# Kernel optimization log

Hardware: AMD Instinct MI355X
Metric: run time of the kernel (lower is better)

Reference implementation:

```python
import jax, jax.numpy as jnp
import numpy as np
import math

B, L, DIM = 2, 2048, 2048
N_HEADS, N_KV = 16, 4
HD = DIM // N_HEADS          # 128
N_REP = N_HEADS // N_KV      # 4
THETA = 10000.0


def setup_inputs() -> dict:
    key = jax.random.key(0)
    ks = jax.random.split(key, 6)
    x = jax.random.normal(ks[0], (B, L, DIM), dtype=jnp.float32)
    # rotary phasor freqs_cis = exp(i * t * inv_freq), stored as cos/sin
    inv_freq = 1.0 / (THETA ** (jnp.arange(0, HD, 2, dtype=jnp.float32) / HD))  # [HD//2]
    ang = jnp.arange(L, dtype=jnp.float32)[:, None] * inv_freq[None, :]          # [L, HD//2]
    freqs_cos = jnp.cos(ang)
    freqs_sin = jnp.sin(ang)
    s = 0.02
    wq = jax.random.normal(ks[1], (DIM, DIM), dtype=jnp.float32) * s
    wk = jax.random.normal(ks[2], (N_KV * HD, DIM), dtype=jnp.float32) * s
    wv = jax.random.normal(ks[3], (N_KV * HD, DIM), dtype=jnp.float32) * s
    wo = jax.random.normal(ks[4], (DIM, DIM), dtype=jnp.float32) * s
    return {"x": x, "freqs_cos": freqs_cos, "freqs_sin": freqs_sin,
            "wq": wq, "wk": wk, "wv": wv, "wo": wo}


def _apply_rope(t, cos, sin):
    # t: [B, L, H, HD]; cos/sin: [L, HD//2] -> broadcast [1, L, 1, HD//2]
    tr = t.reshape(*t.shape[:-1], HD // 2, 2)
    t0, t1 = tr[..., 0], tr[..., 1]
    c = cos[None, :, None, :]
    s = sin[None, :, None, :]
    r0 = t0 * c - t1 * s
    r1 = t0 * s + t1 * c
    return jnp.stack([r0, r1], axis=-1).reshape(t.shape)


def reference(x, freqs_cos, freqs_sin, wq, wk, wv, wo):
    Bx, Lx, _ = x.shape
    xq = (x @ wq.T).reshape(Bx, Lx, N_HEADS, HD)
    xk = (x @ wk.T).reshape(Bx, Lx, N_KV, HD)
    xv = (x @ wv.T).reshape(Bx, Lx, N_KV, HD)
    xq = _apply_rope(xq, freqs_cos, freqs_sin)
    xk = _apply_rope(xk, freqs_cos, freqs_sin)
    # repeat_kv (GQA expansion) then [B, H, L, HD]
    keys = jnp.repeat(xk, N_REP, axis=2).transpose(0, 2, 1, 3)
    values = jnp.repeat(xv, N_REP, axis=2).transpose(0, 2, 1, 3)
    q = xq.transpose(0, 2, 1, 3)
    scores = jnp.einsum('bhqd,bhkd->bhqk', q, keys) / math.sqrt(HD)
    mask = jnp.triu(jnp.full((Lx, Lx), -jnp.inf, dtype=scores.dtype), k=1)
    scores = scores + mask[None, None]
    probs = jax.nn.softmax(scores.astype(jnp.float32), axis=-1).astype(q.dtype)
    out = jnp.einsum('bhqk,bhkd->bhqd', probs, values)
    out = out.transpose(0, 2, 1, 3).reshape(Bx, Lx, -1)
    output = out @ wo.T
    return (output, keys, values)
```

## Files before the change

kernel.cpp:

```cpp
#include <hip/hip_runtime.h>
#include <hip/hip_bf16.h>

using bf16x8 = __attribute__((ext_vector_type(8))) short;
using f32x4  = __attribute__((ext_vector_type(4))) float;

__device__ __forceinline__ unsigned short f32_to_bf16(float f) {
  unsigned u = __float_as_uint(f);
  u += 0x7FFFu + ((u >> 16) & 1u);
  return (unsigned short)(u >> 16);
}
__device__ __forceinline__ unsigned pack2(float lo, float hi) {
  __hip_bfloat162 h = __float22bfloat162_rn(make_float2(lo, hi));
  return *reinterpret_cast<unsigned*>(&h);
}
__device__ __forceinline__ void gload_lds16(const void* g, void* l) {
  __builtin_amdgcn_global_load_lds(
      (const __attribute__((address_space(1))) unsigned int*)g,
      (__attribute__((address_space(3))) unsigned int*)l, 16, 0, 0);
}

__global__ void cast_bf16_kernel(const float* __restrict__ src,
                                 unsigned short* __restrict__ dst) {
  int i = blockIdx.x * blockDim.x + threadIdx.x;
  float4 v = reinterpret_cast<const float4*>(src)[i];
  ushort4 o;
  o.x = f32_to_bf16(v.x); o.y = f32_to_bf16(v.y);
  o.z = f32_to_bf16(v.z); o.w = f32_to_bf16(v.w);
  reinterpret_cast<ushort4*>(dst)[i] = o;
}
__global__ void cast2_bf16_kernel(const float* __restrict__ s0, unsigned short* __restrict__ d0,
                                  int n0v, const float* __restrict__ s1,
                                  unsigned short* __restrict__ d1) {
  int i = blockIdx.x * blockDim.x + threadIdx.x;
  const float* s; unsigned short* d; int j;
  if (i < n0v) { s = s0; d = d0; j = i; } else { s = s1; d = d1; j = i - n0v; }
  float4 v = reinterpret_cast<const float4*>(s)[j];
  ushort4 o;
  o.x = f32_to_bf16(v.x); o.y = f32_to_bf16(v.y);
  o.z = f32_to_bf16(v.z); o.w = f32_to_bf16(v.w);
  reinterpret_cast<ushort4*>(d)[j] = o;
}

template <int BM>
__global__ __launch_bounds__(512, 2) void gemm256_kernel(
    const unsigned short* __restrict__ A, const unsigned short* __restrict__ Bw,
    float* __restrict__ C, int M, int N, int K) {
  constexpr int ABYTES = BM * 128;
  constexpr int BBYTES = 256 * 128;
  constexpr int BUFB   = ABYTES + BBYTES;
  constexpr int ALOADS = BM / 64;
  constexpr int WROWS  = BM / 32;
  __shared__ __align__(16) char Lsh[2 * BUFB];

  const int tid = threadIdx.x;
  const int wid = tid >> 6, lane = tid & 63;
  const int lr = lane & 15, lg = lane >> 4;
  const int wr = wid >> 2, wc = wid & 3;
  const int bn = blockIdx.x, bm = blockIdx.y;
  const int x0 = lg * 16;

  f32x4 acc[WROWS][4] = {};

  const char* Ag = (const char*)A + (size_t)(bm * BM) * K * 2;
  const char* Bg = (const char*)Bw + (size_t)(bn * 256) * K * 2;

  int aoff[ALOADS], boff[4];
#pragma unroll
  for (int i = 0; i < ALOADS; ++i) {
    int lin = wid * (BM * 16) + i * 1024 + lane * 16;
    int grow = lin >> 7;
    int gcol = (lin & 127) ^ ((grow & 7) << 4);
    aoff[i] = grow * (K * 2) + gcol;
  }
#pragma unroll
  for (int i = 0; i < 4; ++i) {
    int lin = wid * 4096 + i * 1024 + lane * 16;
    int grow = lin >> 7;
    int gcol = (lin & 127) ^ ((grow & 7) << 4);
    boff[i] = grow * (K * 2) + gcol;
  }

  auto stage = [&](int s, int buf) {
    const int kb = s * 128;
    char* Lb = Lsh + buf * BUFB;
#pragma unroll
    for (int i = 0; i < ALOADS; ++i)
      gload_lds16(Ag + aoff[i] + kb, Lb + wid * (BM * 16) + i * 1024);
#pragma unroll
    for (int i = 0; i < 4; ++i)
      gload_lds16(Bg + boff[i] + kb, Lb + ABYTES + wid * 4096 + i * 1024);
  };

  auto kstep = [&](char* Lb) {
    bf16x8 bfr[4][2];
#pragma unroll
    for (int fc = 0; fc < 4; ++fc) {
      const int row = wc * 64 + fc * 16 + lr;
      const int base = ABYTES + row * 128;
      const int sw = (row & 7) << 4;
#pragma unroll
      for (int ks = 0; ks < 2; ++ks)
        bfr[fc][ks] = *reinterpret_cast<const bf16x8*>(Lb + base + ((ks * 64 + x0) ^ sw));
    }
#pragma unroll
    for (int q = 0; q < WROWS / 2; ++q) {
      bf16x8 af[2][2];
#pragma unroll
      for (int t = 0; t < 2; ++t) {
        const int row = wr * (BM / 2) + (2 * q + t) * 16 + lr;
        const int base = row * 128;
        const int sw = (row & 7) << 4;
#pragma unroll
        for (int ks = 0; ks < 2; ++ks)
          af[t][ks] = *reinterpret_cast<const bf16x8*>(Lb + base + ((ks * 64 + x0) ^ sw));
      }
      asm volatile("s_waitcnt lgkmcnt(0)" ::: "memory");
      __builtin_amdgcn_sched_barrier(0);
      __builtin_amdgcn_s_setprio(1);
#pragma unroll
      for (int t = 0; t < 2; ++t)
#pragma unroll
        for (int fc = 0; fc < 4; ++fc) {
          acc[2 * q + t][fc] = __builtin_amdgcn_mfma_f32_16x16x32_bf16(af[t][0], bfr[fc][0], acc[2 * q + t][fc], 0, 0, 0);
          acc[2 * q + t][fc] = __builtin_amdgcn_mfma_f32_16x16x32_bf16(af[t][1], bfr[fc][1], acc[2 * q + t][fc], 0, 0, 0);
        }
      __builtin_amdgcn_s_setprio(0);
    }
  };

  const int NST = K >> 6;
  stage(0, 0);
  for (int it = 0; it < NST / 2; ++it) {
    __builtin_amdgcn_s_barrier();
    stage(2 * it + 1, 1);
    if constexpr (BM == 256) asm volatile("s_waitcnt vmcnt(8)" ::: "memory");
    else                     asm volatile("s_waitcnt vmcnt(6)" ::: "memory");
    __builtin_amdgcn_s_barrier();
    kstep(Lsh);
    __builtin_amdgcn_s_barrier();
    if (it < NST / 2 - 1) {
      stage(2 * it + 2, 0);
      if constexpr (BM == 256) asm volatile("s_waitcnt vmcnt(8)" ::: "memory");
      else                     asm volatile("s_waitcnt vmcnt(6)" ::: "memory");
    } else {
      asm volatile("s_waitcnt vmcnt(0)" ::: "memory");
    }
    __builtin_amdgcn_s_barrier();
    kstep(Lsh + BUFB);
  }

#pragma unroll
  for (int fr = 0; fr < WROWS; ++fr) {
    const int m = bm * BM + wr * (BM / 2) + fr * 16 + lg * 4;
#pragma unroll
    for (int fc = 0; fc < 4; ++fc) {
      const int n = bn * 256 + wc * 64 + fc * 16 + lr;
#pragma unroll
      for (int r = 0; r < 4; ++r)
        C[(size_t)(m + r) * N + n] = acc[fr][fc][r];
    }
  }
}

__global__ void rope_k_kernel(const float* __restrict__ xqkv, const float* __restrict__ fc,
                              const float* __restrict__ fs, unsigned short* __restrict__ kbf,
                              float* __restrict__ keys) {
  int idx = blockIdx.x * 256 + threadIdx.x;
  int i = idx & 63;
  int kvh = (idx >> 6) & 3;
  int l = (idx >> 8) & 2047;
  int b = idx >> 19;
  float2 t = reinterpret_cast<const float2*>(xqkv)[(size_t)(b * 2048 + l) * 1536 + 1024 + kvh * 64 + i];
  float c = fc[l * 64 + i], s = fs[l * 64 + i];
  float r0 = t.x * c - t.y * s;
  float r1 = t.x * s + t.y * c;
  int kidx = ((b * 4 + kvh) * 2048 + l) * 64 + i;
  ushort2 o; o.x = f32_to_bf16(r0); o.y = f32_to_bf16(r1);
  reinterpret_cast<ushort2*>(kbf)[kidx] = o;
  float2 f; f.x = r0; f.y = r1;
#pragma unroll
  for (int rep = 0; rep < 4; ++rep) {
    int h = kvh * 4 + rep;
    reinterpret_cast<float2*>(keys)[((b * 16 + h) * 2048 + l) * 64 + i] = f;
  }
}

__global__ void v_proc_kernel(const float* __restrict__ xqkv, unsigned short* __restrict__ vt,
                              float* __restrict__ values) {
  int idx = blockIdx.x * 256 + threadIdx.x;
  int d = idx & 127;
  int kvh = (idx >> 7) & 3;
  int l = (idx >> 9) & 2047;
  int b = idx >> 20;
  float v = xqkv[(size_t)(b * 2048 + l) * 3072 + 2560 + kvh * 128 + d];
#pragma unroll
  for (int rep = 0; rep < 4; ++rep) {
    int h = kvh * 4 + rep;
    values[((size_t)(b * 16 + h) * 2048 + l) * 128 + d] = v;
  }
  vt[((size_t)(b * 4 + kvh) * 128 + d) * 2048 + l] = f32_to_bf16(v);
}

__global__ __launch_bounds__(256) void attn_kernel(
    const float* __restrict__ xq, const float* __restrict__ fc,
    const float* __restrict__ fs, const unsigned short* __restrict__ kbf,
    const unsigned short* __restrict__ vt, unsigned short* __restrict__ obf) {
  __shared__ unsigned short Ks[64 * 128];
  __shared__ unsigned short Vs[128 * 64];
  const int tid = threadIdx.x;
  const int w = tid >> 6, lane = tid & 63;
  const int lr = lane & 15, lg = lane >> 4;
  const int bid = blockIdx.x;
  const int qt = 15 - (bid >> 5);
  const int bh = bid & 31;
  const int b = bh >> 4, h = bh & 15, kv = h >> 2;
  const float ALPHA = 0.12751791437664778f;
  const int swz = (lr & 7) << 4;

  const int qr0 = qt * 128 + w * 16 + lr;
  const int qr1 = qr0 + 64;

  bf16x8 qf[2][4];
#pragma unroll
  for (int t = 0; t < 2; ++t) {
    const int qrow = t ? qr1 : qr0;
    const float* xqp = xq + (size_t)(b * 2048 + qrow) * 3072 + h * 128;
    const float* fcp = fc + qrow * 64;
    const float* fsp = fs + qrow * 64;
#pragma unroll
    for (int s = 0; s < 4; ++s) {
      float4 f0 = *reinterpret_cast<const float4*>(xqp + s * 32 + lg * 8);
      float4 f1 = *reinterpret_cast<const float4*>(xqp + s * 32 + lg * 8 + 4);
      float4 c4 = *reinterpret_cast<const float4*>(fcp + s * 16 + lg * 4);
      float4 s4 = *reinterpret_cast<const float4*>(fsp + s * 16 + lg * 4);
      c4.x *= ALPHA; c4.y *= ALPHA; c4.z *= ALPHA; c4.w *= ALPHA;
      s4.x *= ALPHA; s4.y *= ALPHA; s4.z *= ALPHA; s4.w *= ALPHA;
      union { bf16x8 v8; unsigned u[4]; } uu;
      uu.u[0] = pack2(f0.x * c4.x - f0.y * s4.x, f0.x * s4.x + f0.y * c4.x);
      uu.u[1] = pack2(f0.z * c4.y - f0.w * s4.y, f0.z * s4.y + f0.w * c4.y);
      uu.u[2] = pack2(f1.x * c4.z - f1.y * s4.z, f1.x * s4.z + f1.y * c4.z);
      uu.u[3] = pack2(f1.z * c4.w - f1.w * s4.w, f1.z * s4.w + f1.w * c4.w);
      qf[t][s] = uu.v8;
    }
  }

  f32x4 acc[2][8] = {};
  float mrow[2] = {-1e30f, -1e30f}, lsum[2] = {0.f, 0.f};

  const char* kgbase = (const char*)(kbf + (size_t)(b * 4 + kv) * 2048 * 128);
  const char* vgbase = (const char*)(vt + (size_t)(b * 4 + kv) * 128 * 2048);

  int ksrc[4], vsrc[4];
#pragma unroll
  for (int i = 0; i < 4; ++i) {
    int p = w * 4096 + i * 1024 + lane * 16;
    int krow = p >> 8;
    int kperm = ((krow >> 5) << 5) + ((krow >> 4) & 1) + (((krow >> 2) & 3) << 3) + ((krow & 3) << 1);
    int kcol = (p & 255) ^ ((krow & 7) << 4);
    ksrc[i] = kperm * 256 + kcol;
    int drow = p >> 7;
    int dcol = (p & 127) ^ ((drow & 7) << 4);
    vsrc[i] = drow * 4096 + dcol;
  }

  auto softmax_t = [&](const f32x4* st, int t, bool mask, int qrow, int kb, bf16x8* pt) {
    float xv[4][4];
    float mt = -1e30f;
#pragma unroll
    for (int c = 0; c < 4; ++c)
#pragma unroll
      for (int r = 0; r < 4; ++r) {
        float v = st[c][r];
        if (mask) {
          int ka = kb + ((c >> 1) << 5) + (c & 1) + 8 * lg + 2 * r;
          v = (ka <= qrow) ? v : -1e30f;
        }
        xv[c][r] = v;
        mt = fmaxf(mt, v);
      }
    mt = fmaxf(mt, __shfl_xor(mt, 16));
    mt = fmaxf(mt, __shfl_xor(mt, 32));
    float facm = 1.0f;
    if (!__all(mt <= mrow[t] + 8.0f)) {
      float mnew = fmaxf(mrow[t], mt);
      facm = exp2f(mrow[t] - mnew);
      mrow[t] = mnew;
#pragma unroll
      for (int dt = 0; dt < 8; ++dt)
#pragma unroll
        for (int r = 0; r < 4; ++r) acc[t][dt][r] *= facm;
    }
    float rs = 0.f;
    float pv[4][4];
#pragma unroll
    for (int c = 0; c < 4; ++c)
#pragma unroll
      for (int r = 0; r < 4; ++r) {
        float p = exp2f(xv[c][r] - mrow[t]);
        pv[c][r] = p;
        rs += p;
      }
    rs += __shfl_xor(rs, 16);
    rs += __shfl_xor(rs, 32);
    lsum[t] = lsum[t] * facm + rs;
#pragma unroll
    for (int kk = 0; kk < 2; ++kk) {
      union { bf16x8 v8; unsigned u[4]; } uu;
#pragma unroll
      for (int wd = 0; wd < 4; ++wd)
        uu.u[wd] = pack2(pv[2 * kk][wd], pv[2 * kk + 1][wd]);
      pt[kk] = uu.v8;
    }
  };

  const int nst = 2 * qt + 2;
  for (int j = 0; j < nst; ++j) {
    const int kb = j * 64;
    __syncthreads();
    {
      const char* kg = kgbase + (size_t)kb * 256;
      const char* vg = vgbase + (size_t)kb * 2;
#pragma unroll
      for (int i = 0; i < 4; ++i) {
        gload_lds16(kg + ksrc[i], (char*)Ks + w * 4096 + i * 1024);
        gload_lds16(vg + vsrc[i], (char*)Vs + w * 4096 + i * 1024);
      }
    }
    __syncthreads();
    const bool only1 = (j == nst - 1);
    const bool do0 = !only1;
    const bool m0 = (j == nst - 2);
    const bool m1 = only1;
    f32x4 sT0[4], sT1[4];
#pragma unroll
    for (int c = 0; c < 4; ++c) {
      bf16x8 kf[4];
#pragma unroll
      for (int s = 0; s < 4; ++s)
        kf[s] = *reinterpret_cast<const bf16x8*>((char*)Ks + (((c * 16 + lr) * 256 + s * 64 + lg * 16) ^ swz));
      f32x4 t0 = {0.f, 0.f, 0.f, 0.f}, t1 = {0.f, 0.f, 0.f, 0.f};
#pragma unroll
      for (int s = 0; s < 4; ++s) {
        if (do0) t0 = __builtin_amdgcn_mfma_f32_16x16x32_bf16(kf[s], qf[0][s], t0, 0, 0, 0);
        t1 = __builtin_amdgcn_mfma_f32_16x16x32_bf16(kf[s], qf[1][s], t1, 0, 0, 0);
      }
      sT0[c] = t0; sT1[c] = t1;
    }
    bf16x8 pt0[2], pt1[2];
    if (do0) softmax_t(sT0, 0, m0, qr0, kb, pt0);
    softmax_t(sT1, 1, m1, qr1, kb, pt1);
#pragma unroll
    for (int dt = 0; dt < 8; ++dt) {
      bf16x8 v0 = *reinterpret_cast<const bf16x8*>((char*)Vs + (((dt * 16 + lr) * 128 + lg * 16) ^ swz));
      bf16x8 v1 = *reinterpret_cast<const bf16x8*>((char*)Vs + (((dt * 16 + lr) * 128 + 64 + lg * 16) ^ swz));
      if (do0) {
        acc[0][dt] = __builtin_amdgcn_mfma_f32_16x16x32_bf16(v0, pt0[0], acc[0][dt], 0, 0, 0);
        acc[0][dt] = __builtin_amdgcn_mfma_f32_16x16x32_bf16(v1, pt0[1], acc[0][dt], 0, 0, 0);
      }
      acc[1][dt] = __builtin_amdgcn_mfma_f32_16x16x32_bf16(v0, pt1[0], acc[1][dt], 0, 0, 0);
      acc[1][dt] = __builtin_amdgcn_mfma_f32_16x16x32_bf16(v1, pt1[1], acc[1][dt], 0, 0, 0);
    }
  }

#pragma unroll
  for (int t = 0; t < 2; ++t) {
    const int qrow = t ? qr1 : qr0;
    float inv = 1.0f / lsum[t];
#pragma unroll
    for (int dt = 0; dt < 8; ++dt) {
      ushort4 o;
      o.x = f32_to_bf16(acc[t][dt][0] * inv);
      o.y = f32_to_bf16(acc[t][dt][1] * inv);
      o.z = f32_to_bf16(acc[t][dt][2] * inv);
      o.w = f32_to_bf16(acc[t][dt][3] * inv);
      *reinterpret_cast<ushort4*>(obf + ((size_t)(b * 2048 + qrow)) * 2048 + h * 128 + dt * 16 + lg * 4) = o;
    }
  }
}

extern "C" void kernel_launch(void* const* d_in, const int* in_sizes, int n_in,
                              void* d_out, int out_size, void* d_ws, size_t ws_size,
                              hipStream_t stream) {
  const float* x  = (const float*)d_in[0];
  const float* fc = (const float*)d_in[1];
  const float* fs = (const float*)d_in[2];
  const float* wq = (const float*)d_in[3];
  const float* wk = (const float*)d_in[4];
  const float* wv = (const float*)d_in[5];
  const float* wo = (const float*)d_in[6];

  float* out    = (float*)d_out;
  float* keys   = out + 8388608;
  float* values = out + 16777216;

  char* ws = (char*)d_ws;
  unsigned short* WQKV = (unsigned short*)(ws + 0);
  unsigned short* WO   = (unsigned short*)(ws + 12582912);
  unsigned short* XBF  = (unsigned short*)(ws + 20971520);
  float*          XQKV = (float*)(ws + 37748736);
  unsigned short* KBF  = (unsigned short*)(ws + 88080384);
  unsigned short* VTB  = (unsigned short*)(ws + 92274688);
  unsigned short* ATT  = XBF;

  cast2_bf16_kernel<<<8192, 256, 0, stream>>>(wq, WQKV, 1048576, wo, WO);
  cast2_bf16_kernel<<<2048, 256, 0, stream>>>(wk, WQKV + 2048 * 2048, 262144,
                                              wv, WQKV + 2560 * 2048);
  cast_bf16_kernel<<<8192, 256, 0, stream>>>(x, XBF);

  gemm256_kernel<256><<<dim3(12, 16), 512, 0, stream>>>(XBF, WQKV, XQKV, 4096, 3072, 2048);

  rope_k_kernel<<<4096, 256, 0, stream>>>(XQKV, fc, fs, KBF, keys);
  v_proc_kernel<<<8192, 256, 0, stream>>>(XQKV, VTB, values);

  attn_kernel<<<512, 256, 0, stream>>>(XQKV, fc, fs, KBF, VTB, ATT);

  gemm256_kernel<128><<<dim3(8, 32), 512, 0, stream>>>(ATT, WO, out, 4096, 2048, 2048);
}
```

Measured before the change: 265.5 us.

## Fuse cast and KV-prep launches; restructure attention to read K/V directly from global

```diff
diff --git a/kernel.cpp b/kernel.cpp
--- a/kernel.cpp
+++ b/kernel.cpp
@@ -19,26 +19,24 @@
       (__attribute__((address_space(3))) unsigned int*)l, 16, 0, 0);
 }
 
-__global__ void cast_bf16_kernel(const float* __restrict__ src,
-                                 unsigned short* __restrict__ dst) {
+__global__ void cast_all_kernel(const float* __restrict__ wq, const float* __restrict__ wo,
+                                const float* __restrict__ wk, const float* __restrict__ wv,
+                                const float* __restrict__ x,
+                                unsigned short* __restrict__ WQKV,
+                                unsigned short* __restrict__ WO,
+                                unsigned short* __restrict__ XBF) {
   int i = blockIdx.x * blockDim.x + threadIdx.x;
-  float4 v = reinterpret_cast<const float4*>(src)[i];
+  const float4* s; ushort4* d; int j;
+  if (i < 1048576)      { s = (const float4*)wq; d = (ushort4*)WQKV;            j = i; }
+  else if (i < 2097152) { s = (const float4*)wo; d = (ushort4*)WO;              j = i - 1048576; }
+  else if (i < 2359296) { s = (const float4*)wk; d = (ushort4*)WQKV + 1048576;  j = i - 2097152; }
+  else if (i < 2621440) { s = (const float4*)wv; d = (ushort4*)WQKV + 1310720;  j = i - 2359296; }
+  else                  { s = (const float4*)x;  d = (ushort4*)XBF;             j = i - 2621440; }
+  float4 v = s[j];
   ushort4 o;
   o.x = f32_to_bf16(v.x); o.y = f32_to_bf16(v.y);
   o.z = f32_to_bf16(v.z); o.w = f32_to_bf16(v.w);
-  reinterpret_cast<ushort4*>(dst)[i] = o;
-}
-__global__ void cast2_bf16_kernel(const float* __restrict__ s0, unsigned short* __restrict__ d0,
-                                  int n0v, const float* __restrict__ s1,
-                                  unsigned short* __restrict__ d1) {
-  int i = blockIdx.x * blockDim.x + threadIdx.x;
-  const float* s; unsigned short* d; int j;
-  if (i < n0v) { s = s0; d = d0; j = i; } else { s = s1; d = d1; j = i - n0v; }
-  float4 v = reinterpret_cast<const float4*>(s)[j];
-  ushort4 o;
-  o.x = f32_to_bf16(v.x); o.y = f32_to_bf16(v.y);
-  o.z = f32_to_bf16(v.z); o.w = f32_to_bf16(v.w);
-  reinterpret_cast<ushort4*>(d)[j] = o;
+  d[j] = o;
 }
 
 template <int BM>
@@ -162,68 +160,64 @@
   }
 }
 
-__global__ void rope_k_kernel(const float* __restrict__ xqkv, const float* __restrict__ fc,
-                              const float* __restrict__ fs, unsigned short* __restrict__ kbf,
-                              float* __restrict__ keys) {
-  int idx = blockIdx.x * 256 + threadIdx.x;
-  int i = idx & 63;
-  int kvh = (idx >> 6) & 3;
-  int l = (idx >> 8) & 2047;
-  int b = idx >> 19;
-  float2 t = reinterpret_cast<const float2*>(xqkv)[(size_t)(b * 2048 + l) * 1536 + 1024 + kvh * 64 + i];
-  float c = fc[l * 64 + i], s = fs[l * 64 + i];
-  float r0 = t.x * c - t.y * s;
-  float r1 = t.x * s + t.y * c;
-  int kidx = ((b * 4 + kvh) * 2048 + l) * 64 + i;
-  ushort2 o; o.x = f32_to_bf16(r0); o.y = f32_to_bf16(r1);
-  reinterpret_cast<ushort2*>(kbf)[kidx] = o;
-  float2 f; f.x = r0; f.y = r1;
-#pragma unroll
-  for (int rep = 0; rep < 4; ++rep) {
-    int h = kvh * 4 + rep;
-    reinterpret_cast<float2*>(keys)[((b * 16 + h) * 2048 + l) * 64 + i] = f;
-  }
-}
-
-__global__ void v_proc_kernel(const float* __restrict__ xqkv, unsigned short* __restrict__ vt,
-                              float* __restrict__ values) {
-  int idx = blockIdx.x * 256 + threadIdx.x;
-  int d = idx & 127;
-  int kvh = (idx >> 7) & 3;
-  int l = (idx >> 9) & 2047;
-  int b = idx >> 20;
-  float v = xqkv[(size_t)(b * 2048 + l) * 3072 + 2560 + kvh * 128 + d];
-#pragma unroll
-  for (int rep = 0; rep < 4; ++rep) {
-    int h = kvh * 4 + rep;
-    values[((size_t)(b * 16 + h) * 2048 + l) * 128 + d] = v;
-  }
-  vt[((size_t)(b * 4 + kvh) * 128 + d) * 2048 + l] = f32_to_bf16(v);
+__global__ void kv_proc_kernel(const float* __restrict__ xqkv, const float* __restrict__ fc,
+                               const float* __restrict__ fs, unsigned short* __restrict__ kbf,
+                               float* __restrict__ keys, unsigned short* __restrict__ vt,
+                               float* __restrict__ values) {
+  int bid = blockIdx.x;
+  if (bid < 4096) {
+    int idx = bid * 256 + threadIdx.x;
+    int i = idx & 63;
+    int kvh = (idx >> 6) & 3;
+    int l = (idx >> 8) & 2047;
+    int b = idx >> 19;
+    float2 t = reinterpret_cast<const float2*>(xqkv)[(size_t)(b * 2048 + l) * 1536 + 1024 + kvh * 64 + i];
+    float c = fc[l * 64 + i], s = fs[l * 64 + i];
+    float r0 = t.x * c - t.y * s;
+    float r1 = t.x * s + t.y * c;
+    int kidx = ((b * 4 + kvh) * 2048 + l) * 64 + i;
+    ushort2 o; o.x = f32_to_bf16(r0); o.y = f32_to_bf16(r1);
+    reinterpret_cast<ushort2*>(kbf)[kidx] = o;
+    float2 f; f.x = r0; f.y = r1;
+#pragma unroll
+    for (int rep = 0; rep < 4; ++rep) {
+      int h = kvh * 4 + rep;
+      reinterpret_cast<float2*>(keys)[((b * 16 + h) * 2048 + l) * 64 + i] = f;
+    }
+  } else {
+    int idx = (bid - 4096) * 256 + threadIdx.x;
+    int d = idx & 127;
+    int kvh = (idx >> 7) & 3;
+    int l = (idx >> 9) & 2047;
+    int b = idx >> 20;
+    float v = xqkv[(size_t)(b * 2048 + l) * 3072 + 2560 + kvh * 128 + d];
+#pragma unroll
+    for (int rep = 0; rep < 4; ++rep) {
+      int h = kvh * 4 + rep;
+      values[((size_t)(b * 16 + h) * 2048 + l) * 128 + d] = v;
+    }
+    vt[((size_t)(b * 4 + kvh) * 128 + d) * 2048 + l] = f32_to_bf16(v);
+  }
 }
 
 __global__ __launch_bounds__(256) void attn_kernel(
     const float* __restrict__ xq, const float* __restrict__ fc,
     const float* __restrict__ fs, const unsigned short* __restrict__ kbf,
     const unsigned short* __restrict__ vt, unsigned short* __restrict__ obf) {
-  __shared__ unsigned short Ks[64 * 128];
-  __shared__ unsigned short Vs[128 * 64];
+  __shared__ unsigned short Pbuf[4][16 * 40];
   const int tid = threadIdx.x;
   const int w = tid >> 6, lane = tid & 63;
   const int lr = lane & 15, lg = lane >> 4;
   const int bid = blockIdx.x;
-  const int qt = 15 - (bid >> 5);
+  const int qpos = 31 - (bid >> 5);
   const int bh = bid & 31;
   const int b = bh >> 4, h = bh & 15, kv = h >> 2;
+  const int qbase = qpos * 64 + w * 16;
   const float ALPHA = 0.12751791437664778f;
-  const int swz = (lr & 7) << 4;
-
-  const int qr0 = qt * 128 + w * 16 + lr;
-  const int qr1 = qr0 + 64;
-
-  bf16x8 qf[2][4];
-#pragma unroll
-  for (int t = 0; t < 2; ++t) {
-    const int qrow = t ? qr1 : qr0;
+
+  bf16x8 qf[4];
+  {
+    const int qrow = qbase + lr;
     const float* xqp = xq + (size_t)(b * 2048 + qrow) * 3072 + h * 128;
     const float* fcp = fc + qrow * 64;
     const float* fsp = fs + qrow * 64;
@@ -240,140 +234,105 @@
       uu.u[1] = pack2(f0.z * c4.y - f0.w * s4.y, f0.z * s4.y + f0.w * c4.y);
       uu.u[2] = pack2(f1.x * c4.z - f1.y * s4.z, f1.x * s4.z + f1.y * c4.z);
       uu.u[3] = pack2(f1.z * c4.w - f1.w * s4.w, f1.z * s4.w + f1.w * c4.w);
-      qf[t][s] = uu.v8;
-    }
-  }
-
-  f32x4 acc[2][8] = {};
-  float mrow[2] = {-1e30f, -1e30f}, lsum[2] = {0.f, 0.f};
-
-  const char* kgbase = (const char*)(kbf + (size_t)(b * 4 + kv) * 2048 * 128);
-  const char* vgbase = (const char*)(vt + (size_t)(b * 4 + kv) * 128 * 2048);
-
-  int ksrc[4], vsrc[4];
-#pragma unroll
-  for (int i = 0; i < 4; ++i) {
-    int p = w * 4096 + i * 1024 + lane * 16;
-    int krow = p >> 8;
-    int kperm = ((krow >> 5) << 5) + ((krow >> 4) & 1) + (((krow >> 2) & 3) << 3) + ((krow & 3) << 1);
-    int kcol = (p & 255) ^ ((krow & 7) << 4);
-    ksrc[i] = kperm * 256 + kcol;
-    int drow = p >> 7;
-    int dcol = (p & 127) ^ ((drow & 7) << 4);
-    vsrc[i] = drow * 4096 + dcol;
-  }
-
-  auto softmax_t = [&](const f32x4* st, int t, bool mask, int qrow, int kb, bf16x8* pt) {
-    float xv[4][4];
-    float mt = -1e30f;
-#pragma unroll
-    for (int c = 0; c < 4; ++c)
+      qf[s] = uu.v8;
+    }
+  }
+
+  f32x4 acc[8] = {};
+  float mrow[4], lsum[4];
+#pragma unroll
+  for (int r = 0; r < 4; ++r) { mrow[r] = -1e30f; lsum[r] = 0.0f; }
+
+  const unsigned short* kbase_p = kbf + (size_t)(b * 4 + kv) * 2048 * 128;
+  const unsigned short* vbase_p = vt + (size_t)(b * 4 + kv) * 128 * 2048;
+
+  const int nblocks = (qbase + 47) >> 5;
+  for (int j = 0; j < nblocks; ++j) {
+    const int kb = j * 32;
+    f32x4 s0 = {0.f, 0.f, 0.f, 0.f}, s1 = {0.f, 0.f, 0.f, 0.f};
+    __builtin_amdgcn_s_setprio(1);
+#pragma unroll
+    for (int s = 0; s < 4; ++s) {
+      bf16x8 kf = *reinterpret_cast<const bf16x8*>(kbase_p + (size_t)(kb + lr) * 128 + s * 32 + lg * 8);
+      s0 = __builtin_amdgcn_mfma_f32_16x16x32_bf16(qf[s], kf, s0, 0, 0, 0);
+    }
+#pragma unroll
+    for (int s = 0; s < 4; ++s) {
+      bf16x8 kf = *reinterpret_cast<const bf16x8*>(kbase_p + (size_t)(kb + 16 + lr) * 128 + s * 32 + lg * 8);
+      s1 = __builtin_amdgcn_mfma_f32_16x16x32_bf16(qf[s], kf, s1, 0, 0, 0);
+    }
+    __builtin_amdgcn_s_setprio(0);
+    float v0[4], v1[4], rm[4];
+    bool okall = true;
+#pragma unroll
+    for (int r = 0; r < 4; ++r) {
+      int q = qbase + lg * 4 + r;
+      v0[r] = ((kb + lr) <= q) ? s0[r] : -1e30f;
+      v1[r] = ((kb + 16 + lr) <= q) ? s1[r] : -1e30f;
+      float m = fmaxf(v0[r], v1[r]);
+      m = fmaxf(m, __shfl_xor(m, 1));
+      m = fmaxf(m, __shfl_xor(m, 2));
+      m = fmaxf(m, __shfl_xor(m, 4));
+      m = fmaxf(m, __shfl_xor(m, 8));
+      rm[r] = m;
+      okall = okall && (m <= mrow[r] + 8.0f);
+    }
+    float p0[4], p1[4];
+    if (__all(okall)) {
 #pragma unroll
       for (int r = 0; r < 4; ++r) {
-        float v = st[c][r];
-        if (mask) {
-          int ka = kb + ((c >> 1) << 5) + (c & 1) + 8 * lg + 2 * r;
-          v = (ka <= qrow) ? v : -1e30f;
-        }
-        xv[c][r] = v;
-        mt = fmaxf(mt, v);
+        p0[r] = exp2f(v0[r] - mrow[r]);
+        p1[r] = exp2f(v1[r] - mrow[r]);
+        float rs = p0[r] + p1[r];
+        rs += __shfl_xor(rs, 1);
+        rs += __shfl_xor(rs, 2);
+        rs += __shfl_xor(rs, 4);
+        rs += __shfl_xor(rs, 8);
+        lsum[r] += rs;
       }
-    mt = fmaxf(mt, __shfl_xor(mt, 16));
-    mt = fmaxf(mt, __shfl_xor(mt, 32));
-    float facm = 1.0f;
-    if (!__all(mt <= mrow[t] + 8.0f)) {
-      float mnew = fmaxf(mrow[t], mt);
-      facm = exp2f(mrow[t] - mnew);
-      mrow[t] = mnew;
-#pragma unroll
-      for (int dt = 0; dt < 8; ++dt)
-#pragma unroll
-        for (int r = 0; r < 4; ++r) acc[t][dt][r] *= facm;
-    }
-    float rs = 0.f;
-    float pv[4][4];
-#pragma unroll
-    for (int c = 0; c < 4; ++c)
+    } else {
+      float fac[4];
 #pragma unroll
       for (int r = 0; r < 4; ++r) {
-        float p = exp2f(xv[c][r] - mrow[t]);
-        pv[c][r] = p;
-        rs += p;
+        float mnew = fmaxf(mrow[r], rm[r]);
+        fac[r] = exp2f(mrow[r] - mnew);
+        mrow[r] = mnew;
+        p0[r] = exp2f(v0[r] - mnew);
+        p1[r] = exp2f(v1[r] - mnew);
+        float rs = p0[r] + p1[r];
+        rs += __shfl_xor(rs, 1);
+        rs += __shfl_xor(rs, 2);
+        rs += __shfl_xor(rs, 4);
+        rs += __shfl_xor(rs, 8);
+        lsum[r] = lsum[r] * fac[r] + rs;
       }
-    rs += __shfl_xor(rs, 16);
-    rs += __shfl_xor(rs, 32);
-    lsum[t] = lsum[t] * facm + rs;
-#pragma unroll
-    for (int kk = 0; kk < 2; ++kk) {
-      union { bf16x8 v8; unsigned u[4]; } uu;
-#pragma unroll
-      for (int wd = 0; wd < 4; ++wd)
-        uu.u[wd] = pack2(pv[2 * kk][wd], pv[2 * kk + 1][wd]);
-      pt[kk] = uu.v8;
-    }
-  };
-
-  const int nst = 2 * qt + 2;
-  for (int j = 0; j < nst; ++j) {
-    const int kb = j * 64;
-    __syncthreads();
-    {
-      const char* kg = kgbase + (size_t)kb * 256;
-      const char* vg = vgbase + (size_t)kb * 2;
-#pragma unroll
-      for (int i = 0; i < 4; ++i) {
-        gload_lds16(kg + ksrc[i], (char*)Ks + w * 4096 + i * 1024);
-        gload_lds16(vg + vsrc[i], (char*)Vs + w * 4096 + i * 1024);
+#pragma unroll
+      for (int ft = 0; ft < 8; ++ft) {
+        acc[ft][0] *= fac[0]; acc[ft][1] *= fac[1];
+        acc[ft][2] *= fac[2]; acc[ft][3] *= fac[3];
       }
     }
-    __syncthreads();
-    const bool only1 = (j == nst - 1);
-    const bool do0 = !only1;
-    const bool m0 = (j == nst - 2);
-    const bool m1 = only1;
-    f32x4 sT0[4], sT1[4];
-#pragma unroll
-    for (int c = 0; c < 4; ++c) {
-      bf16x8 kf[4];
-#pragma unroll
-      for (int s = 0; s < 4; ++s)
-        kf[s] = *reinterpret_cast<const bf16x8*>((char*)Ks + (((c * 16 + lr) * 256 + s * 64 + lg * 16) ^ swz));
-      f32x4 t0 = {0.f, 0.f, 0.f, 0.f}, t1 = {0.f, 0.f, 0.f, 0.f};
-#pragma unroll
-      for (int s = 0; s < 4; ++s) {
-        if (do0) t0 = __builtin_amdgcn_mfma_f32_16x16x32_bf16(kf[s], qf[0][s], t0, 0, 0, 0);
-        t1 = __builtin_amdgcn_mfma_f32_16x16x32_bf16(kf[s], qf[1][s], t1, 0, 0, 0);
-      }
-      sT0[c] = t0; sT1[c] = t1;
-    }
-    bf16x8 pt0[2], pt1[2];
-    if (do0) softmax_t(sT0, 0, m0, qr0, kb, pt0);
-    softmax_t(sT1, 1, m1, qr1, kb, pt1);
-#pragma unroll
-    for (int dt = 0; dt < 8; ++dt) {
-      bf16x8 v0 = *reinterpret_cast<const bf16x8*>((char*)Vs + (((dt * 16 + lr) * 128 + lg * 16) ^ swz));
-      bf16x8 v1 = *reinterpret_cast<const bf16x8*>((char*)Vs + (((dt * 16 + lr) * 128 + 64 + lg * 16) ^ swz));
-      if (do0) {
-        acc[0][dt] = __builtin_amdgcn_mfma_f32_16x16x32_bf16(v0, pt0[0], acc[0][dt], 0, 0, 0);
-        acc[0][dt] = __builtin_amdgcn_mfma_f32_16x16x32_bf16(v1, pt0[1], acc[0][dt], 0, 0, 0);
-      }
-      acc[1][dt] = __builtin_amdgcn_mfma_f32_16x16x32_bf16(v0, pt1[0], acc[1][dt], 0, 0, 0);
-      acc[1][dt] = __builtin_amdgcn_mfma_f32_16x16x32_bf16(v1, pt1[1], acc[1][dt], 0, 0, 0);
-    }
-  }
-
-#pragma unroll
-  for (int t = 0; t < 2; ++t) {
-    const int qrow = t ? qr1 : qr0;
-    float inv = 1.0f / lsum[t];
-#pragma unroll
-    for (int dt = 0; dt < 8; ++dt) {
-      ushort4 o;
-      o.x = f32_to_bf16(acc[t][dt][0] * inv);
-      o.y = f32_to_bf16(acc[t][dt][1] * inv);
-      o.z = f32_to_bf16(acc[t][dt][2] * inv);
-      o.w = f32_to_bf16(acc[t][dt][3] * inv);
-      *reinterpret_cast<ushort4*>(obf + ((size_t)(b * 2048 + qrow)) * 2048 + h * 128 + dt * 16 + lg * 4) = o;
+#pragma unroll
+    for (int r = 0; r < 4; ++r) {
+      Pbuf[w][(lg * 4 + r) * 40 + lr]      = f32_to_bf16(p0[r]);
+      Pbuf[w][(lg * 4 + r) * 40 + 16 + lr] = f32_to_bf16(p1[r]);
+    }
+    asm volatile("s_waitcnt lgkmcnt(0)" ::: "memory");
+    bf16x8 pa = *reinterpret_cast<const bf16x8*>(&Pbuf[w][lr * 40 + lg * 8]);
+    __builtin_amdgcn_s_setprio(1);
+#pragma unroll
+    for (int ft = 0; ft < 8; ++ft) {
+      bf16x8 vf = *reinterpret_cast<const bf16x8*>(vbase_p + (size_t)(ft * 16 + lr) * 2048 + kb + lg * 8);
+      acc[ft] = __builtin_amdgcn_mfma_f32_16x16x32_bf16(pa, vf, acc[ft], 0, 0, 0);
+    }
+    __builtin_amdgcn_s_setprio(0);
+  }
+#pragma unroll
+  for (int ft = 0; ft < 8; ++ft) {
+#pragma unroll
+    for (int r = 0; r < 4; ++r) {
+      float o = acc[ft][r] / lsum[r];
+      obf[((size_t)(b * 2048 + qbase + lg * 4 + r)) * 2048 + h * 128 + ft * 16 + lr] = f32_to_bf16(o);
     }
   }
 }
@@ -402,17 +361,13 @@
   unsigned short* VTB  = (unsigned short*)(ws + 92274688);
   unsigned short* ATT  = XBF;
 
-  cast2_bf16_kernel<<<8192, 256, 0, stream>>>(wq, WQKV, 1048576, wo, WO);
-  cast2_bf16_kernel<<<2048, 256, 0, stream>>>(wk, WQKV + 2048 * 2048, 262144,
-                                              wv, WQKV + 2560 * 2048);
-  cast_bf16_kernel<<<8192, 256, 0, stream>>>(x, XBF);
+  cast_all_kernel<<<18432, 256, 0, stream>>>(wq, wo, wk, wv, x, WQKV, WO, XBF);
 
   gemm256_kernel<256><<<dim3(12, 16), 512, 0, stream>>>(XBF, WQKV, XQKV, 4096, 3072, 2048);
 
-  rope_k_kernel<<<4096, 256, 0, stream>>>(XQKV, fc, fs, KBF, keys);
-  v_proc_kernel<<<8192, 256, 0, stream>>>(XQKV, VTB, values);
-
-  attn_kernel<<<512, 256, 0, stream>>>(XQKV, fc, fs, KBF, VTB, ATT);
+  kv_proc_kernel<<<12288, 256, 0, stream>>>(XQKV, fc, fs, KBF, keys, VTB, values);
+
+  attn_kernel<<<1024, 256, 0, stream>>>(XQKV, fc, fs, KBF, VTB, ATT);
 
   gemm256_kernel<128><<<dim3(8, 32), 512, 0, stream>>>(ATT, WO, out, 4096, 2048, 2048);
 }
```

Measured after the change: 387.2 us. 45.8% more time.

## Merge cast and KV prep launches; restructure attention softmax through LDS P tile

Applied to the files above, without the earlier changes.

```diff
diff --git a/kernel.cpp b/kernel.cpp
--- a/kernel.cpp
+++ b/kernel.cpp
@@ -19,26 +19,24 @@
       (__attribute__((address_space(3))) unsigned int*)l, 16, 0, 0);
 }
 
-__global__ void cast_bf16_kernel(const float* __restrict__ src,
-                                 unsigned short* __restrict__ dst) {
+__global__ void cast_all_kernel(const float* __restrict__ wq, const float* __restrict__ wo,
+                                const float* __restrict__ wk, const float* __restrict__ wv,
+                                const float* __restrict__ x,
+                                unsigned short* __restrict__ WQKV,
+                                unsigned short* __restrict__ WO,
+                                unsigned short* __restrict__ XBF) {
   int i = blockIdx.x * blockDim.x + threadIdx.x;
-  float4 v = reinterpret_cast<const float4*>(src)[i];
+  const float4* s; ushort4* d; int j;
+  if (i < 1048576)      { s = (const float4*)wq; d = (ushort4*)WQKV;            j = i; }
+  else if (i < 2097152) { s = (const float4*)wo; d = (ushort4*)WO;              j = i - 1048576; }
+  else if (i < 2359296) { s = (const float4*)wk; d = (ushort4*)WQKV + 1048576;  j = i - 2097152; }
+  else if (i < 2621440) { s = (const float4*)wv; d = (ushort4*)WQKV + 1310720;  j = i - 2359296; }
+  else                  { s = (const float4*)x;  d = (ushort4*)XBF;             j = i - 2621440; }
+  float4 v = s[j];
   ushort4 o;
   o.x = f32_to_bf16(v.x); o.y = f32_to_bf16(v.y);
   o.z = f32_to_bf16(v.z); o.w = f32_to_bf16(v.w);
-  reinterpret_cast<ushort4*>(dst)[i] = o;
-}
-__global__ void cast2_bf16_kernel(const float* __restrict__ s0, unsigned short* __restrict__ d0,
-                                  int n0v, const float* __restrict__ s1,
-                                  unsigned short* __restrict__ d1) {
-  int i = blockIdx.x * blockDim.x + threadIdx.x;
-  const float* s; unsigned short* d; int j;
-  if (i < n0v) { s = s0; d = d0; j = i; } else { s = s1; d = d1; j = i - n0v; }
-  float4 v = reinterpret_cast<const float4*>(s)[j];
-  ushort4 o;
-  o.x = f32_to_bf16(v.x); o.y = f32_to_bf16(v.y);
-  o.z = f32_to_bf16(v.z); o.w = f32_to_bf16(v.w);
-  reinterpret_cast<ushort4*>(d)[j] = o;
+  d[j] = o;
 }
 
 template <int BM>
@@ -162,43 +160,44 @@
   }
 }
 
-__global__ void rope_k_kernel(const float* __restrict__ xqkv, const float* __restrict__ fc,
-                              const float* __restrict__ fs, unsigned short* __restrict__ kbf,
-                              float* __restrict__ keys) {
-  int idx = blockIdx.x * 256 + threadIdx.x;
-  int i = idx & 63;
-  int kvh = (idx >> 6) & 3;
-  int l = (idx >> 8) & 2047;
-  int b = idx >> 19;
-  float2 t = reinterpret_cast<const float2*>(xqkv)[(size_t)(b * 2048 + l) * 1536 + 1024 + kvh * 64 + i];
-  float c = fc[l * 64 + i], s = fs[l * 64 + i];
-  float r0 = t.x * c - t.y * s;
-  float r1 = t.x * s + t.y * c;
-  int kidx = ((b * 4 + kvh) * 2048 + l) * 64 + i;
-  ushort2 o; o.x = f32_to_bf16(r0); o.y = f32_to_bf16(r1);
-  reinterpret_cast<ushort2*>(kbf)[kidx] = o;
-  float2 f; f.x = r0; f.y = r1;
-#pragma unroll
-  for (int rep = 0; rep < 4; ++rep) {
-    int h = kvh * 4 + rep;
-    reinterpret_cast<float2*>(keys)[((b * 16 + h) * 2048 + l) * 64 + i] = f;
-  }
-}
-
-__global__ void v_proc_kernel(const float* __restrict__ xqkv, unsigned short* __restrict__ vt,
-                              float* __restrict__ values) {
-  int idx = blockIdx.x * 256 + threadIdx.x;
-  int d = idx & 127;
-  int kvh = (idx >> 7) & 3;
-  int l = (idx >> 9) & 2047;
-  int b = idx >> 20;
-  float v = xqkv[(size_t)(b * 2048 + l) * 3072 + 2560 + kvh * 128 + d];
-#pragma unroll
-  for (int rep = 0; rep < 4; ++rep) {
-    int h = kvh * 4 + rep;
-    values[((size_t)(b * 16 + h) * 2048 + l) * 128 + d] = v;
-  }
-  vt[((size_t)(b * 4 + kvh) * 128 + d) * 2048 + l] = f32_to_bf16(v);
+__global__ void kv_proc_kernel(const float* __restrict__ xqkv, const float* __restrict__ fc,
+                               const float* __restrict__ fs, unsigned short* __restrict__ kbf,
+                               float* __restrict__ keys, unsigned short* __restrict__ vt,
+                               float* __restrict__ values) {
+  int bid = blockIdx.x;
+  if (bid < 4096) {
+    int idx = bid * 256 + threadIdx.x;
+    int i = idx & 63;
+    int kvh = (idx >> 6) & 3;
+    int l = (idx >> 8) & 2047;
+    int b = idx >> 19;
+    float2 t = reinterpret_cast<const float2*>(xqkv)[(size_t)(b * 2048 + l) * 1536 + 1024 + kvh * 64 + i];
+    float c = fc[l * 64 + i], s = fs[l * 64 + i];
+    float r0 = t.x * c - t.y * s;
+    float r1 = t.x * s + t.y * c;
+    int kidx = ((b * 4 + kvh) * 2048 + l) * 64 + i;
+    ushort2 o; o.x = f32_to_bf16(r0); o.y = f32_to_bf16(r1);
+    reinterpret_cast<ushort2*>(kbf)[kidx] = o;
+    float2 f; f.x = r0; f.y = r1;
+#pragma unroll
+    for (int rep = 0; rep < 4; ++rep) {
+      int h = kvh * 4 + rep;
+      reinterpret_cast<float2*>(keys)[((b * 16 + h) * 2048 + l) * 64 + i] = f;
+    }
+  } else {
+    int idx = (bid - 4096) * 256 + threadIdx.x;
+    int d = idx & 127;
+    int kvh = (idx >> 7) & 3;
+    int l = (idx >> 9) & 2047;
+    int b = idx >> 20;
+    float v = xqkv[(size_t)(b * 2048 + l) * 3072 + 2560 + kvh * 128 + d];
+#pragma unroll
+    for (int rep = 0; rep < 4; ++rep) {
+      int h = kvh * 4 + rep;
+      values[((size_t)(b * 16 + h) * 2048 + l) * 128 + d] = v;
+    }
+    vt[((size_t)(b * 4 + kvh) * 128 + d) * 2048 + l] = f32_to_bf16(v);
+  }
 }
 
 __global__ __launch_bounds__(256) void attn_kernel(
@@ -207,6 +206,7 @@
     const unsigned short* __restrict__ vt, unsigned short* __restrict__ obf) {
   __shared__ unsigned short Ks[64 * 128];
   __shared__ unsigned short Vs[128 * 64];
+  __shared__ unsigned short Ps[4][2][16 * 72];
   const int tid = threadIdx.x;
   const int w = tid >> 6, lane = tid & 63;
   const int lr = lane & 15, lg = lane >> 4;
@@ -214,16 +214,14 @@
   const int qt = 15 - (bid >> 5);
   const int bh = bid & 31;
   const int b = bh >> 4, h = bh & 15, kv = h >> 2;
-  const float ALPHA = 0.12751791437664778f;
+  const int q0 = qt * 128 + w * 32;
+  const float ALPHA = 0.08838834764831845f;
   const int swz = (lr & 7) << 4;
 
-  const int qr0 = qt * 128 + w * 16 + lr;
-  const int qr1 = qr0 + 64;
-
   bf16x8 qf[2][4];
 #pragma unroll
   for (int t = 0; t < 2; ++t) {
-    const int qrow = t ? qr1 : qr0;
+    const int qrow = q0 + t * 16 + lr;
     const float* xqp = xq + (size_t)(b * 2048 + qrow) * 3072 + h * 128;
     const float* fcp = fc + qrow * 64;
     const float* fsp = fs + qrow * 64;
@@ -250,88 +248,22 @@
   const char* kgbase = (const char*)(kbf + (size_t)(b * 4 + kv) * 2048 * 128);
   const char* vgbase = (const char*)(vt + (size_t)(b * 4 + kv) * 128 * 2048);
 
-  int ksrc[4], vsrc[4];
-#pragma unroll
-  for (int i = 0; i < 4; ++i) {
-    int p = w * 4096 + i * 1024 + lane * 16;
-    int krow = p >> 8;
-    int kperm = ((krow >> 5) << 5) + ((krow >> 4) & 1) + (((krow >> 2) & 3) << 3) + ((krow & 3) << 1);
-    int kcol = (p & 255) ^ ((krow & 7) << 4);
-    ksrc[i] = kperm * 256 + kcol;
-    int drow = p >> 7;
-    int dcol = (p & 127) ^ ((drow & 7) << 4);
-    vsrc[i] = drow * 4096 + dcol;
-  }
-
-  auto softmax_t = [&](const f32x4* st, int t, bool mask, int qrow, int kb, bf16x8* pt) {
-    float xv[4][4];
-    float mt = -1e30f;
-#pragma unroll
-    for (int c = 0; c < 4; ++c)
-#pragma unroll
-      for (int r = 0; r < 4; ++r) {
-        float v = st[c][r];
-        if (mask) {
-          int ka = kb + ((c >> 1) << 5) + (c & 1) + 8 * lg + 2 * r;
-          v = (ka <= qrow) ? v : -1e30f;
-        }
-        xv[c][r] = v;
-        mt = fmaxf(mt, v);
-      }
-    mt = fmaxf(mt, __shfl_xor(mt, 16));
-    mt = fmaxf(mt, __shfl_xor(mt, 32));
-    float facm = 1.0f;
-    if (!__all(mt <= mrow[t] + 8.0f)) {
-      float mnew = fmaxf(mrow[t], mt);
-      facm = exp2f(mrow[t] - mnew);
-      mrow[t] = mnew;
-#pragma unroll
-      for (int dt = 0; dt < 8; ++dt)
-#pragma unroll
-        for (int r = 0; r < 4; ++r) acc[t][dt][r] *= facm;
-    }
-    float rs = 0.f;
-    float pv[4][4];
-#pragma unroll
-    for (int c = 0; c < 4; ++c)
-#pragma unroll
-      for (int r = 0; r < 4; ++r) {
-        float p = exp2f(xv[c][r] - mrow[t]);
-        pv[c][r] = p;
-        rs += p;
-      }
-    rs += __shfl_xor(rs, 16);
-    rs += __shfl_xor(rs, 32);
-    lsum[t] = lsum[t] * facm + rs;
-#pragma unroll
-    for (int kk = 0; kk < 2; ++kk) {
-      union { bf16x8 v8; unsigned u[4]; } uu;
-#pragma unroll
-      for (int wd = 0; wd < 4; ++wd)
-        uu.u[wd] = pack2(pv[2 * kk][wd], pv[2 * kk + 1][wd]);
-      pt[kk] = uu.v8;
-    }
-  };
-
-  const int nst = 2 * qt + 2;
-  for (int j = 0; j < nst; ++j) {
+  const int nblocks = 2 * qt + 2;
+  for (int j = 0; j < nblocks; ++j) {
     const int kb = j * 64;
     __syncthreads();
-    {
-      const char* kg = kgbase + (size_t)kb * 256;
-      const char* vg = vgbase + (size_t)kb * 2;
-#pragma unroll
-      for (int i = 0; i < 4; ++i) {
-        gload_lds16(kg + ksrc[i], (char*)Ks + w * 4096 + i * 1024);
-        gload_lds16(vg + vsrc[i], (char*)Vs + w * 4096 + i * 1024);
-      }
+#pragma unroll
+    for (int i = 0; i < 4; ++i) {
+      int p = w * 4096 + i * 1024 + lane * 16;
+      int krow = p >> 8;
+      int kcol = (p & 255) ^ ((krow & 7) << 4);
+      gload_lds16(kgbase + (size_t)(kb + krow) * 256 + kcol, (char*)Ks + w * 4096 + i * 1024);
+      int drow = p >> 7;
+      int dcol = (p & 127) ^ ((drow & 7) << 4);
+      gload_lds16(vgbase + (size_t)drow * 4096 + (size_t)kb * 2 + dcol, (char*)Vs + w * 4096 + i * 1024);
     }
     __syncthreads();
-    const bool only1 = (j == nst - 1);
-    const bool do0 = !only1;
-    const bool m0 = (j == nst - 2);
-    const bool m1 = only1;
-    f32x4 sT0[4], sT1[4];
+    f32x4 sT[2][4];
 #pragma unroll
     for (int c = 0; c < 4; ++c) {
       bf16x8 kf[4];
@@ -341,30 +273,75 @@
       f32x4 t0 = {0.f, 0.f, 0.f, 0.f}, t1 = {0.f, 0.f, 0.f, 0.f};
 #pragma unroll
       for (int s = 0; s < 4; ++s) {
-        if (do0) t0 = __builtin_amdgcn_mfma_f32_16x16x32_bf16(kf[s], qf[0][s], t0, 0, 0, 0);
+        t0 = __builtin_amdgcn_mfma_f32_16x16x32_bf16(kf[s], qf[0][s], t0, 0, 0, 0);
         t1 = __builtin_amdgcn_mfma_f32_16x16x32_bf16(kf[s], qf[1][s], t1, 0, 0, 0);
       }
-      sT0[c] = t0; sT1[c] = t1;
-    }
-    bf16x8 pt0[2], pt1[2];
-    if (do0) softmax_t(sT0, 0, m0, qr0, kb, pt0);
-    softmax_t(sT1, 1, m1, qr1, kb, pt1);
+      sT[0][c] = t0; sT[1][c] = t1;
+    }
+#pragma unroll
+    for (int t = 0; t < 2; ++t) {
+      const int qrow = q0 + t * 16 + lr;
+      float x[4][4];
+      float mt = -1e30f;
+#pragma unroll
+      for (int c = 0; c < 4; ++c)
+#pragma unroll
+        for (int r = 0; r < 4; ++r) {
+          int k = kb + c * 16 + lg * 4 + r;
+          float v = (k <= qrow) ? sT[t][c][r] : -1e30f;
+          x[c][r] = v;
+          mt = fmaxf(mt, v);
+        }
+      mt = fmaxf(mt, __shfl_xor(mt, 16));
+      mt = fmaxf(mt, __shfl_xor(mt, 32));
+      float mnew = fmaxf(mrow[t], mt);
+      float fac = __expf(mrow[t] - mnew);
+      mrow[t] = mnew;
+      float rs = 0.f;
+      unsigned pw[4][2];
+#pragma unroll
+      for (int c = 0; c < 4; ++c)
+#pragma unroll
+        for (int j2 = 0; j2 < 2; ++j2) {
+          float p0 = __expf(x[c][2 * j2] - mnew);
+          float p1 = __expf(x[c][2 * j2 + 1] - mnew);
+          rs += p0 + p1;
+          pw[c][j2] = pack2(p0, p1);
+        }
+      rs += __shfl_xor(rs, 16);
+      rs += __shfl_xor(rs, 32);
+      lsum[t] = lsum[t] * fac + rs;
+#pragma unroll
+      for (int dt = 0; dt < 8; ++dt)
+#pragma unroll
+        for (int r = 0; r < 4; ++r) acc[t][dt][r] *= fac;
+      char* pb = (char*)&Ps[w][t][0];
+#pragma unroll
+      for (int c = 0; c < 4; ++c)
+#pragma unroll
+        for (int j2 = 0; j2 < 2; ++j2)
+          *reinterpret_cast<unsigned*>(pb + lr * 144 + c * 32 + lg * 8 + j2 * 4) = pw[c][j2];
+    }
+    asm volatile("s_waitcnt lgkmcnt(0)" ::: "memory");
+    __builtin_amdgcn_sched_barrier(0);
+    bf16x8 pt[2][2];
+#pragma unroll
+    for (int t = 0; t < 2; ++t)
+#pragma unroll
+      for (int kk = 0; kk < 2; ++kk)
+        pt[t][kk] = *reinterpret_cast<const bf16x8*>((char*)&Ps[w][t][0] + lr * 144 + kk * 64 + lg * 16);
 #pragma unroll
     for (int dt = 0; dt < 8; ++dt) {
       bf16x8 v0 = *reinterpret_cast<const bf16x8*>((char*)Vs + (((dt * 16 + lr) * 128 + lg * 16) ^ swz));
       bf16x8 v1 = *reinterpret_cast<const bf16x8*>((char*)Vs + (((dt * 16 + lr) * 128 + 64 + lg * 16) ^ swz));
-      if (do0) {
-        acc[0][dt] = __builtin_amdgcn_mfma_f32_16x16x32_bf16(v0, pt0[0], acc[0][dt], 0, 0, 0);
-        acc[0][dt] = __builtin_amdgcn_mfma_f32_16x16x32_bf16(v1, pt0[1], acc[0][dt], 0, 0, 0);
-      }
-      acc[1][dt] = __builtin_amdgcn_mfma_f32_16x16x32_bf16(v0, pt1[0], acc[1][dt], 0, 0, 0);
-      acc[1][dt] = __builtin_amdgcn_mfma_f32_16x16x32_bf16(v1, pt1[1], acc[1][dt], 0, 0, 0);
-    }
-  }
-
+      acc[0][dt] = __builtin_amdgcn_mfma_f32_16x16x32_bf16(v0, pt[0][0], acc[0][dt], 0, 0, 0);
+      acc[0][dt] = __builtin_amdgcn_mfma_f32_16x16x32_bf16(v1, pt[0][1], acc[0][dt], 0, 0, 0);
+      acc[1][dt] = __builtin_amdgcn_mfma_f32_16x16x32_bf16(v0, pt[1][0], acc[1][dt], 0, 0, 0);
+      acc[1][dt] = __builtin_amdgcn_mfma_f32_16x16x32_bf16(v1, pt[1][1], acc[1][dt], 0, 0, 0);
+    }
+  }
 #pragma unroll
   for (int t = 0; t < 2; ++t) {
-    const int qrow = t ? qr1 : qr0;
     float inv = 1.0f / lsum[t];
 #pragma unroll
     for (int dt = 0; dt < 8; ++dt) {
@@ -373,7 +350,7 @@
       o.y = f32_to_bf16(acc[t][dt][1] * inv);
       o.z = f32_to_bf16(acc[t][dt][2] * inv);
       o.w = f32_to_bf16(acc[t][dt][3] * inv);
-      *reinterpret_cast<ushort4*>(obf + ((size_t)(b * 2048 + qrow)) * 2048 + h * 128 + dt * 16 + lg * 4) = o;
+      *reinterpret_cast<ushort4*>(obf + ((size_t)(b * 2048 + q0 + t * 16 + lr)) * 2048 + h * 128 + dt * 16 + lg * 4) = o;
     }
   }
 }
@@ -402,15 +379,11 @@
   unsigned short* VTB  = (unsigned short*)(ws + 92274688);
   unsigned short* ATT  = XBF;
 
-  cast2_bf16_kernel<<<8192, 256, 0, stream>>>(wq, WQKV, 1048576, wo, WO);
-  cast2_bf16_kernel<<<2048, 256, 0, stream>>>(wk, WQKV + 2048 * 2048, 262144,
-                                              wv, WQKV + 2560 * 2048);
-  cast_bf16_kernel<<<8192, 256, 0, stream>>>(x, XBF);
+  cast_all_kernel<<<18432, 256, 0, stream>>>(wq, wo, wk, wv, x, WQKV, WO, XBF);
 
   gemm256_kernel<256><<<dim3(12, 16), 512, 0, stream>>>(XBF, WQKV, XQKV, 4096, 3072, 2048);
 
-  rope_k_kernel<<<4096, 256, 0, stream>>>(XQKV, fc, fs, KBF, keys);
-  v_proc_kernel<<<8192, 256, 0, stream>>>(XQKV, VTB, values);
+  kv_proc_kernel<<<12288, 256, 0, stream>>>(XQKV, fc, fs, KBF, keys, VTB, values);
 
   attn_kernel<<<512, 256, 0, stream>>>(XQKV, fc, fs, KBF, VTB, ATT);
 
```

Measured after the change: 234.2 us. 11.8% less time.
